# Kernel optimization log

Measured on AMD Instinct MI355X. Metric: run time of the kernel, lower is better.

## Reference

```python
import jax, jax.numpy as jnp
import numpy as np
from jax import lax

FP = 64   # frame side
DP = 28   # digit template side
CP = FP - DP + 1  # 37, valid correlation output side


def setup_inputs() -> dict:
    key = jax.random.key(0)
    ks = jax.random.split(key, 6)
    B, T, S, H = 128, 16, 10, 256
    frames = jax.random.normal(ks[0], (B, T, FP, FP), dtype=jnp.float32)
    digit_images = jax.random.uniform(ks[1], (S, B, DP, DP), dtype=jnp.float32)
    W1 = jax.random.normal(ks[2], (CP * CP, H), dtype=jnp.float32) * (1.0 / np.sqrt(CP * CP))
    b1 = jnp.zeros((H,), dtype=jnp.float32)
    W2 = jax.random.normal(ks[3], (H, 2), dtype=jnp.float32) * (1.0 / np.sqrt(H))
    b2 = jnp.zeros((2,), dtype=jnp.float32)
    where_std = jnp.ones((2,), dtype=jnp.float32) * 0.1
    return {"frames": frames, "digit_images": digit_images, "S": S,
            "W1": W1, "b1": b1, "W2": W2, "b2": b2, "where_std": where_std}


def reference(frames, digit_images, S, W1, b1, W2, b2, where_std):
    B, T = frames.shape[0], frames.shape[1]
    # torch: conv2d(frames.transpose(0,1), digit_images.view(S*B,DP,DP).unsqueeze(1), groups=B)
    # lhs: (T, B, FP, FP) treated as batch=T, channels=B; rhs: (S*B, 1, DP, DP)
    lhs = jnp.transpose(frames, (1, 0, 2, 3))              # (T, B, FP, FP)
    rhs = digit_images.reshape(S * B, 1, DP, DP)           # (S*B, 1, DP, DP)
    convolved = lax.conv_general_dilated(
        lhs, rhs, window_strides=(1, 1), padding='VALID',
        feature_group_count=B,
        dimension_numbers=('NCHW', 'OIHW', 'NCHW'))        # (T, S*B, CP, CP)
    convolved = convolved.reshape(T, S, B, CP * CP)
    hidden = jnp.tanh(convolved @ W1 + b1)                 # (T, S, B, H)
    q_mean = jnp.tanh(hidden @ W2 + b2)                    # (T, S, B, 2)
    q_mean = jnp.transpose(q_mean, (1, 2, 0, 3))           # (S, B, T, 2)
    eps = jax.random.normal(jax.random.key(1), q_mean.shape, dtype=q_mean.dtype)
    z_where = q_mean + where_std * eps                     # Normal(q_mean, std).sample()
    return q_mean, z_where
```

## Files before the change

### kernel.cpp

```cpp
#include <hip/hip_runtime.h>
#include <stdint.h>

#define CROWB 2816
#define NOUT 40960
#define DGB 32832

typedef _Float16 f16x8 __attribute__((ext_vector_type(8)));
typedef float f32x4 __attribute__((ext_vector_type(4)));

#define TF_ROT(x, r) (((x) << (r)) | ((x) >> (32 - (r))))
#define TF_ROUND(r) { x0 += x1; x1 = TF_ROT(x1, (r)); x1 ^= x0; }

__device__ __forceinline__ float erfinv_f(float x) {
  float w = -log1pf(-x * x);
  float p;
  if (w < 5.0f) {
    w -= 2.5f;
    p = 2.81022636e-08f;
    p = fmaf(p, w, 3.43273939e-07f);
    p = fmaf(p, w, -3.5233877e-06f);
    p = fmaf(p, w, -4.39150654e-06f);
    p = fmaf(p, w, 0.00021858087f);
    p = fmaf(p, w, -0.00125372503f);
    p = fmaf(p, w, -0.00417768164f);
    p = fmaf(p, w, 0.246640727f);
    p = fmaf(p, w, 1.50140941f);
  } else {
    w = sqrtf(w) - 3.0f;
    p = -0.000200214257f;
    p = fmaf(p, w, 0.000100950558f);
    p = fmaf(p, w, 0.00134934322f);
    p = fmaf(p, w, -0.00367342844f);
    p = fmaf(p, w, 0.00573950773f);
    p = fmaf(p, w, -0.0076224613f);
    p = fmaf(p, w, 0.00943887047f);
    p = fmaf(p, w, 1.00167406f);
    p = fmaf(p, w, 2.83297682f);
  }
  return p * x;
}

__device__ __forceinline__ float gauss_eps(int p) {
  const unsigned ks0 = 0u, ks1 = 1u, ks2 = 0x1BD11BDBu;
  unsigned x0 = 0u + ks0;
  unsigned x1 = (unsigned)p + ks1;
  TF_ROUND(13) TF_ROUND(15) TF_ROUND(26) TF_ROUND(6)
  x0 += ks1; x1 += ks2 + 1u;
  TF_ROUND(17) TF_ROUND(29) TF_ROUND(16) TF_ROUND(24)
  x0 += ks2; x1 += ks0 + 2u;
  TF_ROUND(13) TF_ROUND(15) TF_ROUND(26) TF_ROUND(6)
  x0 += ks0; x1 += ks1 + 3u;
  TF_ROUND(17) TF_ROUND(29) TF_ROUND(16) TF_ROUND(24)
  x0 += ks1; x1 += ks2 + 4u;
  TF_ROUND(13) TF_ROUND(15) TF_ROUND(26) TF_ROUND(6)
  x0 += ks2; x1 += ks0 + 5u;
  unsigned bits = x0 ^ x1;
  unsigned fb = (bits >> 9) | 0x3f800000u;
  float f = __uint_as_float(fb) - 1.0f;
  const float lo = -0.99999994f;
  float u = f * 2.0f + lo;
  u = fmaxf(lo, u);
  return 1.41421356f * erfinv_f(u);
}

__device__ __forceinline__ float fast_tanh(float x) {
  float e = __expf(2.0f * x);
  return 1.0f - 2.0f * __builtin_amdgcn_rcpf(e + 1.0f);
}

__device__ __forceinline__ uint32_t packh2(float lo, float hi) {
  union { _Float16 h[2]; uint32_t u; } c;
  c.h[0] = (_Float16)lo; c.h[1] = (_Float16)hi;
  return c.u;
}

__global__ __launch_bounds__(256) void prep_w1t(const float* __restrict__ W1,
                                                uint8_t* __restrict__ w1t) {
  int k0 = blockIdx.x * 16;
  int tid = threadIdx.x;
  float v[16];
  #pragma unroll
  for (int r = 0; r < 16; ++r) {
    int k = k0 + r;
    v[r] = (k < 1369) ? W1[(size_t)k * 256 + tid] : 0.0f;
  }
  uint32_t o[8];
  #pragma unroll
  for (int a = 0; a < 8; ++a) o[a] = packh2(v[2*a], v[2*a+1]);
  uint8_t* dst = w1t + (size_t)tid * CROWB + (size_t)k0 * 2;
  *(uint4*)(dst)      = make_uint4(o[0], o[1], o[2], o[3]);
  *(uint4*)(dst + 16) = make_uint4(o[4], o[5], o[6], o[7]);
}

__global__ __launch_bounds__(256, 3) void conv_mfma(
    const float* __restrict__ frames, const float* __restrict__ digits,
    uint8_t* __restrict__ conv_out)
{
  __shared__ __align__(16) uint8_t smem[52992];
  const int g = blockIdx.x >> 4, t = blockIdx.x & 15;
  const int tid = threadIdx.x;
  const int lane = tid & 63, w = tid >> 6;
  const int l15 = lane & 15, lg = lane >> 4;
  const int jo = lg * 8;

  {
    const float* fbase = frames + ((size_t)(g * 16 + t)) * 4096;
    float h[20];
    const float4* f4 = (const float4*)(fbase + tid * 16);
    #pragma unroll
    for (int a = 0; a < 4; ++a) {
      float4 v = f4[a];
      h[4*a] = v.x; h[4*a+1] = v.y; h[4*a+2] = v.z; h[4*a+3] = v.w;
    }
    float t0 = __shfl_down(h[0], 1), t1 = __shfl_down(h[1], 1),
          t2 = __shfl_down(h[2], 1), t3 = __shfl_down(h[3], 1);
    if (lane == 63) {
      int bidx = tid * 16 + 16;
      t0 = (bidx + 0 < 4096) ? fbase[bidx + 0] : 0.0f;
      t1 = (bidx + 1 < 4096) ? fbase[bidx + 1] : 0.0f;
      t2 = (bidx + 2 < 4096) ? fbase[bidx + 2] : 0.0f;
      t3 = (bidx + 3 < 4096) ? fbase[bidx + 3] : 0.0f;
    }
    h[16] = t0; h[17] = t1; h[18] = t2; h[19] = t3;
    #pragma unroll
    for (int c = 0; c < 8; ++c) {
      int cc = (c + tid) & 7;
      int le = 2 * cc;
      uint4 v;
      v.x = packh2(h[le],   h[le+1]);
      v.y = packh2(h[le+2], h[le+3]);
      v.z = packh2(h[le+1], h[le+2]);
      v.w = packh2(h[le+3], h[le+4]);
      *(uint4*)(smem + 128 * tid + 16 * cc) = v;
    }
    if (tid < 16) *(uint32_t*)(smem + 32768 + tid * 4) = 0u;
  }
  {
    uint32_t* dz = (uint32_t*)(smem + DGB);
    for (int q = tid; q < 5040; q += 256) dz[q] = 0u;
  }
  __syncthreads();
  {
    const float* dsrc = digits + (size_t)g * 7840;
    for (int idx = tid; idx < 7840; idx += 256) {
      int s = idx / 784; int r = idx - s * 784;
      int i = r / 28;    int j = r - i * 28;
      *(_Float16*)(smem + DGB + (size_t)(i * 360 + s * 36 + j) * 2) = (_Float16)dsrc[idx];
    }
  }
  __syncthreads();

  uint32_t abase[22];
  #pragma unroll
  for (int j2 = 0; j2 < 22; ++j2) {
    int tile = w + 4 * j2;
    int p = tile * 16 + l15;
    int py = p / 37, px = p - py * 37;
    abase[j2] = (uint32_t)(py * 64 + px + jo) * 8u;
  }
  const int s2 = (l15 < 10) ? l15 : 0;
  const uint32_t bbase = DGB + (uint32_t)(s2 * 36 + jo) * 2u;

  f32x4 acc[22];
  #pragma unroll
  for (int j2 = 0; j2 < 22; ++j2) acc[j2] = (f32x4){0.f, 0.f, 0.f, 0.f};

  for (int i = 0; i < 28; ++i) {
    f16x8 bfrag = *(const f16x8*)(smem + bbase + i * 720);
    #pragma unroll
    for (int j2 = 0; j2 < 22; ++j2) {
      const uint8_t* ap = smem + abase[j2] + i * 512;
      union { uint2 u2[2]; f16x8 v; } A;
      A.u2[0] = *(const uint2*)(ap);
      A.u2[1] = *(const uint2*)(ap + 32);
      acc[j2] = __builtin_amdgcn_mfma_f32_16x16x32_f16(A.v, bfrag, acc[j2], 0, 0, 0);
    }
  }

  if (l15 < 10) {
    size_t rb = ((size_t)t * 1280 + 10 * g + l15) * (size_t)CROWB;
    #pragma unroll
    for (int j2 = 0; j2 < 22; ++j2) {
      int p0 = (w + 4 * j2) * 16 + lg * 4;
      #pragma unroll
      for (int r = 0; r < 4; ++r) {
        int p = p0 + r;
        if (p < 1369)
          *(_Float16*)(conv_out + rb + (size_t)p * 2) = (_Float16)acc[j2][r];
      }
    }
  }
}

__global__ __launch_bounds__(256) void mlp_mfma(
    const uint8_t* __restrict__ conv_out, const uint8_t* __restrict__ w1t,
    const float* __restrict__ b1, const float* __restrict__ W2,
    const float* __restrict__ b2, const float* __restrict__ wstd,
    float* __restrict__ out)
{
  __shared__ __align__(16) uint8_t smem[45568];
  const int tid = threadIdx.x;
  const int lane = tid & 63, w = tid >> 6;
  const int l15 = lane & 15, lg = lane >> 4;
  const int m0 = blockIdx.x * 80;

  int aR[3], ac16[3]; bool av[3];
  #pragma unroll
  for (int it = 0; it < 3; ++it) {
    int q = tid + 256 * it;
    av[it] = (q < 640); aR[it] = q >> 3; ac16[it] = q & 7;
  }
  int bR[8], bc16[8];
  #pragma unroll
  for (int it = 0; it < 8; ++it) {
    int q = tid + 256 * it;
    bR[it] = q >> 3; bc16[it] = q & 7;
  }

  f32x4 acc[5][4];
  #pragma unroll
  for (int mt = 0; mt < 5; ++mt)
    #pragma unroll
    for (int nj = 0; nj < 4; ++nj) acc[mt][nj] = (f32x4){0.f, 0.f, 0.f, 0.f};

  uint4 ra[3], rb[8];
  #pragma unroll
  for (int it = 0; it < 3; ++it)
    if (av[it]) ra[it] = *(const uint4*)(conv_out + (size_t)(m0 + aR[it]) * CROWB + ac16[it] * 16);
  #pragma unroll
  for (int it = 0; it < 8; ++it)
    rb[it] = *(const uint4*)(w1t + (size_t)bR[it] * CROWB + bc16[it] * 16);

  for (int k0 = 0; k0 < 1408; k0 += 64) {
    __syncthreads();
    #pragma unroll
    for (int it = 0; it < 3; ++it)
      if (av[it]) *(uint4*)(smem + aR[it] * 128 + ((ac16[it] * 16) ^ ((aR[it] & 7) << 4))) = ra[it];
    #pragma unroll
    for (int it = 0; it < 8; ++it)
      *(uint4*)(smem + 10240 + bR[it] * 128 + ((bc16[it] * 16) ^ ((bR[it] & 7) << 4))) = rb[it];
    __syncthreads();
    if (k0 + 64 < 1408) {
      #pragma unroll
      for (int it = 0; it < 3; ++it)
        if (av[it]) ra[it] = *(const uint4*)(conv_out + (size_t)(m0 + aR[it]) * CROWB + (size_t)(k0 + 64) * 2 + ac16[it] * 16);
      #pragma unroll
      for (int it = 0; it < 8; ++it)
        rb[it] = *(const uint4*)(w1t + (size_t)bR[it] * CROWB + (size_t)(k0 + 64) * 2 + bc16[it] * 16);
    }
    #pragma unroll
    for (int q = 0; q < 2; ++q) {
      f16x8 bf[4];
      #pragma unroll
      for (int nj = 0; nj < 4; ++nj) {
        int h = (w * 4 + nj) * 16 + l15;
        bf[nj] = *(const f16x8*)(smem + 10240 + h * 128 + ((q * 64 + lg * 16) ^ ((h & 7) << 4)));
      }
      #pragma unroll
      for (int mt = 0; mt < 5; ++mt) {
        int R = mt * 16 + l15;
        union { uint4 u; f16x8 v; } A;
        A.u = *(const uint4*)(smem + R * 128 + ((q * 64 + lg * 16) ^ ((R & 7) << 4)));
        #pragma unroll
        for (int nj = 0; nj < 4; ++nj)
          acc[mt][nj] = __builtin_amdgcn_mfma_f32_16x16x32_f16(A.v, bf[nj], acc[mt][nj], 0, 0, 0);
      }
    }
  }

  float qp[5][4][2];
  #pragma unroll
  for (int mt = 0; mt < 5; ++mt)
    #pragma unroll
    for (int r = 0; r < 4; ++r) { qp[mt][r][0] = 0.f; qp[mt][r][1] = 0.f; }

  #pragma unroll
  for (int nj = 0; nj < 4; ++nj) {
    int h = (w * 4 + nj) * 16 + l15;
    float bb = b1[h];
    float w20 = W2[2 * h], w21 = W2[2 * h + 1];
    #pragma unroll
    for (int mt = 0; mt < 5; ++mt)
      #pragma unroll
      for (int r = 0; r < 4; ++r) {
        float hid = fast_tanh(acc[mt][nj][r] + bb);
        qp[mt][r][0] = fmaf(hid, w20, qp[mt][r][0]);
        qp[mt][r][1] = fmaf(hid, w21, qp[mt][r][1]);
      }
  }
  #pragma unroll
  for (int off = 1; off <= 8; off <<= 1) {
    #pragma unroll
    for (int mt = 0; mt < 5; ++mt)
      #pragma unroll
      for (int r = 0; r < 4; ++r) {
        qp[mt][r][0] += __shfl_xor(qp[mt][r][0], off);
        qp[mt][r][1] += __shfl_xor(qp[mt][r][1], off);
      }
  }
  float* qb = (float*)(smem + 43008);
  if (l15 == 0) {
    #pragma unroll
    for (int mt = 0; mt < 5; ++mt)
      #pragma unroll
      for (int r = 0; r < 4; ++r) {
        int row = mt * 16 + lg * 4 + r;
        qb[(w * 80 + row) * 2 + 0] = qp[mt][r][0];
        qb[(w * 80 + row) * 2 + 1] = qp[mt][r][1];
      }
  }
  __syncthreads();
  if (tid < 160) {
    int row = tid >> 1, c = tid & 1;
    float sum = qb[row * 2 + c] + qb[(80 + row) * 2 + c] +
                qb[(160 + row) * 2 + c] + qb[(240 + row) * 2 + c];
    float q = fast_tanh(sum + b2[c]);
    int m = m0 + row;
    int tt = m / 1280;
    int o = m - tt * 1280;
    int base = (o * 16 + tt) * 2;
    out[base + c] = q;
    out[NOUT + base + c] = q + wstd[c] * gauss_eps(base + c);
  }
}

extern "C" void kernel_launch(void* const* d_in, const int* in_sizes, int n_in,
                              void* d_out, int out_size, void* d_ws, size_t ws_size,
                              hipStream_t stream) {
  const float* frames = (const float*)d_in[0];
  const float* digits = (const float*)d_in[1];
  const float* W1   = (const float*)d_in[3];
  const float* b1   = (const float*)d_in[4];
  const float* W2   = (const float*)d_in[5];
  const float* b2   = (const float*)d_in[6];
  const float* wstd = (const float*)d_in[7];
  uint8_t* conv_ws = (uint8_t*)d_ws;
  uint8_t* w1t     = conv_ws + (size_t)20480 * CROWB;
  float* out = (float*)d_out;

  prep_w1t<<<dim3(88), dim3(256), 0, stream>>>(W1, w1t);
  conv_mfma<<<dim3(2048), dim3(256), 0, stream>>>(frames, digits, conv_ws);
  mlp_mfma<<<dim3(256), dim3(256), 0, stream>>>(conv_ws, w1t, b1, W2, b2, wstd, out);
}
```

Before: 315.3 us.

## Double-buffer MLP GEMM LDS tiles and widen block to eight waves

Rewrites the MLP GEMM main loop to use double-buffered LDS tiles with a K-step of 32 and a single barrier per iteration. Rows are padded to 80 bytes instead of using the XOR swizzle. The block grows from 256 to 512 threads, so each wave computes two N-tiles instead of four, and the final reduction sums eight wave partials. This aims to overlap global loads with MFMA work and raise waves per CU, at the cost of more LDS, more iterations and more barriers.

```diff
diff --git a/kernel.cpp b/kernel.cpp
--- a/kernel.cpp
+++ b/kernel.cpp
@@ -192,80 +192,92 @@
   }
 }
 
-__global__ __launch_bounds__(256) void mlp_mfma(
+#define ABUF 6400
+#define BBUF 20480
+#define BBASE0 12800
+#define QBOFF 53760
+__global__ __launch_bounds__(512) void mlp_mfma(
     const uint8_t* __restrict__ conv_out, const uint8_t* __restrict__ w1t,
     const float* __restrict__ b1, const float* __restrict__ W2,
     const float* __restrict__ b2, const float* __restrict__ wstd,
     float* __restrict__ out)
 {
-  __shared__ __align__(16) uint8_t smem[45568];
+  __shared__ __align__(16) uint8_t smem[58880];
   const int tid = threadIdx.x;
   const int lane = tid & 63, w = tid >> 6;
   const int l15 = lane & 15, lg = lane >> 4;
   const int m0 = blockIdx.x * 80;
 
-  int aR[3], ac16[3]; bool av[3];
+  int soff[3];
+  int sbump[3];
+  const uint8_t* sg[3];
   #pragma unroll
   for (int it = 0; it < 3; ++it) {
-    int q = tid + 256 * it;
-    av[it] = (q < 640); aR[it] = q >> 3; ac16[it] = q & 7;
-  }
-  int bR[8], bc16[8];
-  #pragma unroll
-  for (int it = 0; it < 8; ++it) {
-    int q = tid + 256 * it;
-    bR[it] = q >> 3; bc16[it] = q & 7;
-  }
-
-  f32x4 acc[5][4];
-  #pragma unroll
-  for (int mt = 0; mt < 5; ++mt)
-    #pragma unroll
-    for (int nj = 0; nj < 4; ++nj) acc[mt][nj] = (f32x4){0.f, 0.f, 0.f, 0.f};
-
-  uint4 ra[3], rb[8];
+    int q = tid + 512 * it;
+    if (q < 320) {
+      int R = q >> 2, c = q & 3;
+      soff[it] = R * 80 + c * 16;
+      sbump[it] = ABUF;
+      sg[it] = conv_out + (size_t)(m0 + R) * CROWB + c * 16;
+    } else if (q < 1344) {
+      int q2 = q - 320; int h = q2 >> 2, c = q2 & 3;
+      soff[it] = BBASE0 + h * 80 + c * 16;
+      sbump[it] = BBUF;
+      sg[it] = w1t + (size_t)h * CROWB + c * 16;
+    } else {
+      soff[it] = -1; sbump[it] = 0; sg[it] = conv_out;
+    }
+  }
+
+  f32x4 acc[5][2];
+  #pragma unroll
+  for (int mt = 0; mt < 5; ++mt) {
+    acc[mt][0] = (f32x4){0.f, 0.f, 0.f, 0.f};
+    acc[mt][1] = (f32x4){0.f, 0.f, 0.f, 0.f};
+  }
+
+  uint4 rg[3];
   #pragma unroll
   for (int it = 0; it < 3; ++it)
-    if (av[it]) ra[it] = *(const uint4*)(conv_out + (size_t)(m0 + aR[it]) * CROWB + ac16[it] * 16);
-  #pragma unroll
-  for (int it = 0; it < 8; ++it)
-    rb[it] = *(const uint4*)(w1t + (size_t)bR[it] * CROWB + bc16[it] * 16);
-
-  for (int k0 = 0; k0 < 1408; k0 += 64) {
-    __syncthreads();
-    #pragma unroll
-    for (int it = 0; it < 3; ++it)
-      if (av[it]) *(uint4*)(smem + aR[it] * 128 + ((ac16[it] * 16) ^ ((aR[it] & 7) << 4))) = ra[it];
-    #pragma unroll
-    for (int it = 0; it < 8; ++it)
-      *(uint4*)(smem + 10240 + bR[it] * 128 + ((bc16[it] * 16) ^ ((bR[it] & 7) << 4))) = rb[it];
-    __syncthreads();
-    if (k0 + 64 < 1408) {
+    if (soff[it] >= 0) rg[it] = *(const uint4*)(sg[it]);
+  #pragma unroll
+  for (int it = 0; it < 3; ++it)
+    if (soff[it] >= 0) *(uint4*)(smem + soff[it]) = rg[it];
+  __syncthreads();
+
+  for (int kt = 0; kt < 44; ++kt) {
+    const int cur = kt & 1;
+    const bool more = (kt + 1 < 44);
+    if (more) {
       #pragma unroll
       for (int it = 0; it < 3; ++it)
-        if (av[it]) ra[it] = *(const uint4*)(conv_out + (size_t)(m0 + aR[it]) * CROWB + (size_t)(k0 + 64) * 2 + ac16[it] * 16);
-      #pragma unroll
-      for (int it = 0; it < 8; ++it)
-        rb[it] = *(const uint4*)(w1t + (size_t)bR[it] * CROWB + (size_t)(k0 + 64) * 2 + bc16[it] * 16);
-    }
-    #pragma unroll
-    for (int q = 0; q < 2; ++q) {
-      f16x8 bf[4];
-      #pragma unroll
-      for (int nj = 0; nj < 4; ++nj) {
-        int h = (w * 4 + nj) * 16 + l15;
-        bf[nj] = *(const f16x8*)(smem + 10240 + h * 128 + ((q * 64 + lg * 16) ^ ((h & 7) << 4)));
+        if (soff[it] >= 0) rg[it] = *(const uint4*)(sg[it] + (size_t)(kt + 1) * 64);
+    }
+    {
+      const uint8_t* aB = smem + (cur ? ABUF : 0);
+      const uint8_t* bB = smem + BBASE0 + (cur ? BBUF : 0);
+      f16x8 bf[2];
+      #pragma unroll
+      for (int nj = 0; nj < 2; ++nj) {
+        int h = (w * 2 + nj) * 16 + l15;
+        bf[nj] = *(const f16x8*)(bB + h * 80 + lg * 16);
       }
       #pragma unroll
       for (int mt = 0; mt < 5; ++mt) {
         int R = mt * 16 + l15;
         union { uint4 u; f16x8 v; } A;
-        A.u = *(const uint4*)(smem + R * 128 + ((q * 64 + lg * 16) ^ ((R & 7) << 4)));
-        #pragma unroll
-        for (int nj = 0; nj < 4; ++nj)
-          acc[mt][nj] = __builtin_amdgcn_mfma_f32_16x16x32_f16(A.v, bf[nj], acc[mt][nj], 0, 0, 0);
-      }
-    }
+        A.u = *(const uint4*)(aB + R * 80 + lg * 16);
+        acc[mt][0] = __builtin_amdgcn_mfma_f32_16x16x32_f16(A.v, bf[0], acc[mt][0], 0, 0, 0);
+        acc[mt][1] = __builtin_amdgcn_mfma_f32_16x16x32_f16(A.v, bf[1], acc[mt][1], 0, 0, 0);
+      }
+    }
+    if (more) {
+      int nxt = (kt + 1) & 1;
+      #pragma unroll
+      for (int it = 0; it < 3; ++it)
+        if (soff[it] >= 0) *(uint4*)(smem + soff[it] + (nxt ? sbump[it] : 0)) = rg[it];
+    }
+    __syncthreads();
   }
 
   float qp[5][4][2];
@@ -275,8 +287,8 @@
     for (int r = 0; r < 4; ++r) { qp[mt][r][0] = 0.f; qp[mt][r][1] = 0.f; }
 
   #pragma unroll
-  for (int nj = 0; nj < 4; ++nj) {
-    int h = (w * 4 + nj) * 16 + l15;
+  for (int nj = 0; nj < 2; ++nj) {
+    int h = (w * 2 + nj) * 16 + l15;
     float bb = b1[h];
     float w20 = W2[2 * h], w21 = W2[2 * h + 1];
     #pragma unroll
@@ -298,7 +310,7 @@
         qp[mt][r][1] += __shfl_xor(qp[mt][r][1], off);
       }
   }
-  float* qb = (float*)(smem + 43008);
+  float* qb = (float*)(smem + QBOFF);
   if (l15 == 0) {
     #pragma unroll
     for (int mt = 0; mt < 5; ++mt)
@@ -312,8 +324,9 @@
   __syncthreads();
   if (tid < 160) {
     int row = tid >> 1, c = tid & 1;
-    float sum = qb[row * 2 + c] + qb[(80 + row) * 2 + c] +
-                qb[(160 + row) * 2 + c] + qb[(240 + row) * 2 + c];
+    float sum = 0.f;
+    #pragma unroll
+    for (int ww = 0; ww < 8; ++ww) sum += qb[(ww * 80 + row) * 2 + c];
     float q = fast_tanh(sum + b2[c]);
     int m = m0 + row;
     int tt = m / 1280;
@@ -340,5 +353,5 @@
 
   prep_w1t<<<dim3(88), dim3(256), 0, stream>>>(W1, w1t);
   conv_mfma<<<dim3(2048), dim3(256), 0, stream>>>(frames, digits, conv_ws);
-  mlp_mfma<<<dim3(256), dim3(256), 0, stream>>>(conv_ws, w1t, b1, W2, b2, wstd, out);
-}
+  mlp_mfma<<<dim3(256), dim3(512), 0, stream>>>(conv_ws, w1t, b1, W2, b2, wstd, out);
+}
```

Result: no change. 310.9 us (-1.4%).

## Shrink MLP GEMM row tile to 32 and drop register prefetch

Applied to the files above, without the earlier changes.

The MLP GEMM kernel now processes 32 rows per block instead of 80, launching 640 blocks rather than 256 so all CUs get work. The register double-buffered prefetch of the next K tile is removed, and loads are issued directly before the LDS stores each iteration. This lowers register and LDS use and should raise occupancy. The cost is that the W1 tile is re-read by more blocks, and global load latency is no longer hidden behind the MFMA work.

```diff
diff --git a/kernel.cpp b/kernel.cpp
--- a/kernel.cpp
+++ b/kernel.cpp
@@ -198,66 +198,43 @@
     const float* __restrict__ b2, const float* __restrict__ wstd,
     float* __restrict__ out)
 {
-  __shared__ __align__(16) uint8_t smem[45568];
+  __shared__ __align__(16) uint8_t smem[37888];
   const int tid = threadIdx.x;
   const int lane = tid & 63, w = tid >> 6;
   const int l15 = lane & 15, lg = lane >> 4;
-  const int m0 = blockIdx.x * 80;
-
-  int aR[3], ac16[3]; bool av[3];
-  #pragma unroll
-  for (int it = 0; it < 3; ++it) {
-    int q = tid + 256 * it;
-    av[it] = (q < 640); aR[it] = q >> 3; ac16[it] = q & 7;
-  }
-  int bR[8], bc16[8];
-  #pragma unroll
-  for (int it = 0; it < 8; ++it) {
-    int q = tid + 256 * it;
-    bR[it] = q >> 3; bc16[it] = q & 7;
-  }
-
-  f32x4 acc[5][4];
-  #pragma unroll
-  for (int mt = 0; mt < 5; ++mt)
+  const int m0 = blockIdx.x * 32;
+
+  f32x4 acc[2][4];
+  #pragma unroll
+  for (int mt = 0; mt < 2; ++mt)
     #pragma unroll
     for (int nj = 0; nj < 4; ++nj) acc[mt][nj] = (f32x4){0.f, 0.f, 0.f, 0.f};
 
-  uint4 ra[3], rb[8];
-  #pragma unroll
-  for (int it = 0; it < 3; ++it)
-    if (av[it]) ra[it] = *(const uint4*)(conv_out + (size_t)(m0 + aR[it]) * CROWB + ac16[it] * 16);
-  #pragma unroll
-  for (int it = 0; it < 8; ++it)
-    rb[it] = *(const uint4*)(w1t + (size_t)bR[it] * CROWB + bc16[it] * 16);
+  const int aR = tid >> 3, ac16 = tid & 7;
 
   for (int k0 = 0; k0 < 1408; k0 += 64) {
     __syncthreads();
-    #pragma unroll
-    for (int it = 0; it < 3; ++it)
-      if (av[it]) *(uint4*)(smem + aR[it] * 128 + ((ac16[it] * 16) ^ ((aR[it] & 7) << 4))) = ra[it];
-    #pragma unroll
-    for (int it = 0; it < 8; ++it)
-      *(uint4*)(smem + 10240 + bR[it] * 128 + ((bc16[it] * 16) ^ ((bR[it] & 7) << 4))) = rb[it];
+    {
+      uint4 v = *(const uint4*)(conv_out + (size_t)(m0 + aR) * CROWB + (size_t)k0 * 2 + ac16 * 16);
+      *(uint4*)(smem + aR * 128 + ((ac16 * 16) ^ ((aR & 7) << 4))) = v;
+    }
+    #pragma unroll
+    for (int it = 0; it < 8; ++it) {
+      int q = tid + 256 * it; int h = q >> 3, c16 = q & 7;
+      uint4 v = *(const uint4*)(w1t + (size_t)h * CROWB + (size_t)k0 * 2 + c16 * 16);
+      *(uint4*)(smem + 4096 + h * 128 + ((c16 * 16) ^ ((h & 7) << 4))) = v;
+    }
     __syncthreads();
-    if (k0 + 64 < 1408) {
-      #pragma unroll
-      for (int it = 0; it < 3; ++it)
-        if (av[it]) ra[it] = *(const uint4*)(conv_out + (size_t)(m0 + aR[it]) * CROWB + (size_t)(k0 + 64) * 2 + ac16[it] * 16);
-      #pragma unroll
-      for (int it = 0; it < 8; ++it)
-        rb[it] = *(const uint4*)(w1t + (size_t)bR[it] * CROWB + (size_t)(k0 + 64) * 2 + bc16[it] * 16);
-    }
     #pragma unroll
     for (int q = 0; q < 2; ++q) {
       f16x8 bf[4];
       #pragma unroll
       for (int nj = 0; nj < 4; ++nj) {
         int h = (w * 4 + nj) * 16 + l15;
-        bf[nj] = *(const f16x8*)(smem + 10240 + h * 128 + ((q * 64 + lg * 16) ^ ((h & 7) << 4)));
-      }
-      #pragma unroll
-      for (int mt = 0; mt < 5; ++mt) {
+        bf[nj] = *(const f16x8*)(smem + 4096 + h * 128 + ((q * 64 + lg * 16) ^ ((h & 7) << 4)));
+      }
+      #pragma unroll
+      for (int mt = 0; mt < 2; ++mt) {
         int R = mt * 16 + l15;
         union { uint4 u; f16x8 v; } A;
         A.u = *(const uint4*)(smem + R * 128 + ((q * 64 + lg * 16) ^ ((R & 7) << 4)));
@@ -268,9 +245,9 @@
     }
   }
 
-  float qp[5][4][2];
-  #pragma unroll
-  for (int mt = 0; mt < 5; ++mt)
+  float qp[2][4][2];
+  #pragma unroll
+  for (int mt = 0; mt < 2; ++mt)
     #pragma unroll
     for (int r = 0; r < 4; ++r) { qp[mt][r][0] = 0.f; qp[mt][r][1] = 0.f; }
 
@@ -280,7 +257,7 @@
     float bb = b1[h];
     float w20 = W2[2 * h], w21 = W2[2 * h + 1];
     #pragma unroll
-    for (int mt = 0; mt < 5; ++mt)
+    for (int mt = 0; mt < 2; ++mt)
       #pragma unroll
       for (int r = 0; r < 4; ++r) {
         float hid = fast_tanh(acc[mt][nj][r] + bb);
@@ -291,29 +268,29 @@
   #pragma unroll
   for (int off = 1; off <= 8; off <<= 1) {
     #pragma unroll
-    for (int mt = 0; mt < 5; ++mt)
+    for (int mt = 0; mt < 2; ++mt)
       #pragma unroll
       for (int r = 0; r < 4; ++r) {
         qp[mt][r][0] += __shfl_xor(qp[mt][r][0], off);
         qp[mt][r][1] += __shfl_xor(qp[mt][r][1], off);
       }
   }
-  float* qb = (float*)(smem + 43008);
+  float* qb = (float*)(smem + 36864);
   if (l15 == 0) {
     #pragma unroll
-    for (int mt = 0; mt < 5; ++mt)
+    for (int mt = 0; mt < 2; ++mt)
       #pragma unroll
       for (int r = 0; r < 4; ++r) {
         int row = mt * 16 + lg * 4 + r;
-        qb[(w * 80 + row) * 2 + 0] = qp[mt][r][0];
-        qb[(w * 80 + row) * 2 + 1] = qp[mt][r][1];
+        qb[(w * 32 + row) * 2 + 0] = qp[mt][r][0];
+        qb[(w * 32 + row) * 2 + 1] = qp[mt][r][1];
       }
   }
   __syncthreads();
-  if (tid < 160) {
+  if (tid < 64) {
     int row = tid >> 1, c = tid & 1;
-    float sum = qb[row * 2 + c] + qb[(80 + row) * 2 + c] +
-                qb[(160 + row) * 2 + c] + qb[(240 + row) * 2 + c];
+    float sum = qb[row * 2 + c] + qb[(32 + row) * 2 + c] +
+                qb[(64 + row) * 2 + c] + qb[(96 + row) * 2 + c];
     float q = fast_tanh(sum + b2[c]);
     int m = m0 + row;
     int tt = m / 1280;
@@ -340,5 +317,5 @@
 
   prep_w1t<<<dim3(88), dim3(256), 0, stream>>>(W1, w1t);
   conv_mfma<<<dim3(2048), dim3(256), 0, stream>>>(frames, digits, conv_ws);
-  mlp_mfma<<<dim3(256), dim3(256), 0, stream>>>(conv_ws, w1t, b1, W2, b2, wstd, out);
-}
+  mlp_mfma<<<dim3(640), dim3(256), 0, stream>>>(conv_ws, w1t, b1, W2, b2, wstd, out);
+}
```

Result: faster. 260.3 us (-17.4%).
